# Kernel tuning notes

Measured on AMD Instinct MI355X. Metric: run time of the kernel, lower is better.

The kernel has to match this reference:

```python
import jax, jax.numpy as jnp
import numpy as np

WS = [1024, 2048, 4096, 8192]
RS = [1, 2, 4, 8]
HEAD_IDX = 0
B, N, C, H = 4, 8192, 1024, 128


def setup_inputs() -> dict:
    key = jax.random.key(0)
    kx, kq, kk, kv = jax.random.split(key, 4)
    x = jax.random.normal(kx, (B, N, C), dtype=jnp.float32)
    # small init scale keeps exp(logits) well-conditioned, like trained weights
    Wq = jax.random.normal(kq, (C, H), dtype=jnp.float32) * 0.02
    Wk = jax.random.normal(kk, (C, H), dtype=jnp.float32) * 0.02
    Wv = jax.random.normal(kv, (C, H), dtype=jnp.float32) * 0.02
    return {"x": x, "Wq": Wq, "Wk": Wk, "Wv": Wv}


def _cfg_attention(x, Wq, Wk, Wv, w, r, offset):
    # one (window, dilation) config: strided gather -> causal attn per segment
    b, n, c = x.shape
    h = Wq.shape[1]
    S = n // w
    xs = x.reshape(b, S, w, c)[:, :, offset::r, :]  # [b,S,m,c] dilated sub-seqs
    m = xs.shape[2]
    q = jnp.einsum('bsmc,ch->bsmh', xs, Wq)
    k = jnp.einsum('bsmc,ch->bsmh', xs, Wk)
    v = jnp.einsum('bsmc,ch->bsmh', xs, Wv)
    scores = jnp.einsum('bsqh,bskh->bsqk', q, k) / jnp.sqrt(jnp.float32(h))
    causal = jnp.tril(jnp.ones((m, m), dtype=bool))
    scores = jnp.where(causal, scores, -jnp.inf)
    lse = jax.scipy.special.logsumexp(scores, axis=-1)       # [b,S,m]
    p = jnp.exp(scores - lse[..., None])                     # stable softmax
    o = jnp.einsum('bsqk,bskh->bsqh', p, v)                  # [b,S,m,h]
    denom = jnp.exp(lse)                                     # softmax denominator
    pos = (jnp.arange(S)[:, None] * w + offset
           + jnp.arange(m)[None, :] * r).reshape(-1)         # flat positions [S*m]
    return pos, o.reshape(b, S * m, h), denom.reshape(b, S * m)


def reference(x, Wq, Wk, Wv):
    b, n, _ = x.shape
    h = Wq.shape[1]
    denom_sums = jnp.zeros((b, n), dtype=x.dtype)
    cfgs = []
    for w, r in zip(WS, RS):
        offset = HEAD_IDX % r
        pos, o, denom = _cfg_attention(x, Wq, Wk, Wv, w, r, offset)
        denom_sums = denom_sums.at[:, pos].add(denom)  # cross-config denom sum
        cfgs.append((pos, o, denom))
    out = jnp.zeros((b, n, h), dtype=x.dtype)
    for pos, o, denom in cfgs:
        alpha = denom / denom_sums[:, pos]             # [b, S*m]
        out = out.at[:, pos, :].add(o * alpha[:, :, None])
    return out
```

## Files before the change

kernel.cpp:

```cpp
#include <hip/hip_runtime.h>

typedef __attribute__((ext_vector_type(8))) short s16x8;
typedef __attribute__((ext_vector_type(4))) short s16x4;
typedef __attribute__((ext_vector_type(4))) float f32x4;

#define MFMA16(a,b,c) __builtin_amdgcn_mfma_f32_16x16x32_bf16((a),(b),(c),0,0,0)

#define GLOAD_LDS16(g, l) \
    __builtin_amdgcn_global_load_lds((const __attribute__((address_space(1))) void*)(g), \
                                     (__attribute__((address_space(3))) void*)(l), 16, 0, 0)

__device__ __forceinline__ unsigned short f2bf(float f) {
    unsigned u = __builtin_bit_cast(unsigned, f);
    u = (u + 0x7FFFu + ((u >> 16) & 1u)) >> 16;
    return (unsigned short)u;
}

#define MB ((size_t)1 << 20)
#define WT_OFF   ((size_t)0)
#define QKV_OFF  (1*MB)
#define VT0_OFF  (25*MB)
#define VT1_OFF  (33*MB)
#define VT2_OFF  (37*MB)
#define VT3_OFF  (39*MB)
#define KG1_OFF  (40*MB)
#define KG2_OFF  (44*MB)
#define KG3_OFF  (46*MB)
#define O0_OFF   (47*MB)
#define O1_OFF   (63*MB)
#define O2_OFF   (71*MB)
#define O3_OFF   (75*MB)
#define L0_OFF   (77*MB)
#define L1_OFF   (L0_OFF + (size_t)131072)
#define L2_OFF   (L1_OFF + (size_t)65536)
#define L3_OFF   (L2_OFF + (size_t)32768)

__global__ __launch_bounds__(256) void k_wt(const float* __restrict__ Wq, const float* __restrict__ Wk,
                                            const float* __restrict__ Wv, unsigned short* __restrict__ Wt) {
    int id = blockIdx.x * 256 + threadIdx.x;
    int mat = id >> 17;
    int rem = id & 131071;
    int h = rem >> 10, c = rem & 1023;
    const float* W = (mat == 0) ? Wq : (mat == 1) ? Wk : Wv;
    Wt[id] = f2bf(W[c * 128 + h]);
}

__global__ __launch_bounds__(256, 2) void k_qkv(const float* __restrict__ x,
                                                const unsigned short* __restrict__ Wt,
                                                unsigned short* __restrict__ QKV) {
    union SMem {
        struct { float As[64][64]; unsigned short Bs[384][64]; } s;
        unsigned short Cs[64][392];
    };
    __shared__ SMem sm;
    float* Asf = &sm.s.As[0][0];
    unsigned short* Bsu = &sm.s.Bs[0][0];

    const int mt = blockIdx.x;
    const int tid = threadIdx.x, lane = tid & 63, wv = tid >> 6;
    const int quad = lane >> 4, m16 = lane & 15;
    const int wr = wv >> 1, wc = wv & 1;
    const float* xb = x + (size_t)mt * 64 * 1024;

    f32x4 acc[2][12];
#pragma unroll
    for (int i = 0; i < 2; i++)
#pragma unroll
        for (int j = 0; j < 12; j++) acc[i][j] = (f32x4)0.f;

    for (int kk = 0; kk < 1024; kk += 64) {
#pragma unroll
        for (int t = 0; t < 4; t++) {
            int id = wv * 4 + t;
            int row = id * 4 + (lane >> 4);
            int gl = (lane & 15) ^ (row & 7);
            GLOAD_LDS16(xb + (size_t)row * 1024 + kk + gl * 4, (char*)Asf + id * 1024);
        }
#pragma unroll
        for (int t = 0; t < 12; t++) {
            int id = wv * 12 + t;
            int col = id * 8 + (lane >> 3);
            int gl = (lane & 7) ^ (lane >> 3);
            GLOAD_LDS16(Wt + (size_t)col * 1024 + kk + gl * 8, (char*)Bsu + id * 1024);
        }
        __syncthreads();
#pragma unroll
        for (int c32 = 0; c32 < 2; c32++) {
            s16x8 a[2], b[12];
#pragma unroll
            for (int rt = 0; rt < 2; rt++) {
                int row = wr * 32 + rt * 16 + m16;
                int g0 = c32 * 8 + quad * 2;
                float4 lo = *(const float4*)&Asf[row * 64 + ((g0 ^ (row & 7)) << 2)];
                float4 hi = *(const float4*)&Asf[row * 64 + (((g0 + 1) ^ (row & 7)) << 2)];
                s16x8 av;
                av[0] = (short)f2bf(lo.x); av[1] = (short)f2bf(lo.y);
                av[2] = (short)f2bf(lo.z); av[3] = (short)f2bf(lo.w);
                av[4] = (short)f2bf(hi.x); av[5] = (short)f2bf(hi.y);
                av[6] = (short)f2bf(hi.z); av[7] = (short)f2bf(hi.w);
                a[rt] = av;
            }
#pragma unroll
            for (int ct = 0; ct < 12; ct++) {
                int col = wc * 192 + ct * 16 + m16;
                b[ct] = *(const s16x8*)&Bsu[col * 64 + (((c32 * 4 + quad) ^ (col & 7)) << 3)];
            }
#pragma unroll
            for (int rt = 0; rt < 2; rt++)
#pragma unroll
                for (int ct = 0; ct < 12; ct++) acc[rt][ct] = MFMA16(a[rt], b[ct], acc[rt][ct]);
        }
        __syncthreads();
    }

#pragma unroll
    for (int rt = 0; rt < 2; rt++)
#pragma unroll
        for (int ct = 0; ct < 12; ct++)
#pragma unroll
            for (int rg = 0; rg < 4; rg++)
                sm.Cs[wr * 32 + rt * 16 + quad * 4 + rg][wc * 192 + ct * 16 + m16] = f2bf(acc[rt][ct][rg]);
    __syncthreads();
#pragma unroll
    for (int i = 0; i < 12; i++) {
        int id = tid + 256 * i;
        int row = id / 48, cc = id % 48;
        int col = cc * 8, mat = col >> 7, h = col & 127;
        *(s16x8*)(QKV + (size_t)mat * 4194304 + ((size_t)(mt * 64 + row)) * 128 + h) =
            *(const s16x8*)&sm.Cs[row][col];
    }
}

__device__ __forceinline__ void decode_vt(int bid, int& c, int& b, int& s, int& t8) {
    int base;
    if (bid < 256)      { c = 0; base = 0; }
    else if (bid < 384) { c = 1; base = 256; }
    else if (bid < 448) { c = 2; base = 384; }
    else                { c = 3; base = 448; }
    int rem = bid - base;
    int sh = 6 - c;
    b = rem >> sh;
    int rr = rem & ((1 << sh) - 1);
    s = rr >> 3; t8 = rr & 7;
}

__global__ __launch_bounds__(256) void k_gather(const unsigned short* __restrict__ QKV, char* __restrict__ ws) {
    const unsigned short* K = QKV + (size_t)1 * 4194304;
    const unsigned short* V = QKV + (size_t)2 * 4194304;
    int bid = blockIdx.x, tid = threadIdx.x;
    if (bid < 480) {
        int c, b, s, kb; decode_vt(bid, c, b, s, kb);
        const int S = 8 >> c, r = 1 << c, wseg = 1024 << c;
        const size_t vtoff[4] = {VT0_OFF, VT1_OFF, VT2_OFF, VT3_OFF};
        unsigned short* Vt = (unsigned short*)(ws + vtoff[c]) + ((size_t)(b * S + s)) * 131072;
        int kq8 = tid & 15, hq = tid >> 4;
        int key0 = kb * 128 + kq8 * 8;
        int jt = key0 >> 6, k0 = key0 & 63;
        s16x8 in[8];
#pragma unroll
        for (int i = 0; i < 8; i++) {
            int tok = s * wseg + (key0 + i) * r;
            in[i] = *(const s16x8*)(V + ((size_t)(b * 8192 + tok)) * 128 + hq * 8);
        }
#pragma unroll
        for (int jh = 0; jh < 8; jh++) {
            s16x8 o;
#pragma unroll
            for (int i = 0; i < 8; i++) o[i] = in[i][jh];
            *(s16x8*)(Vt + (size_t)jt * 8192 + (size_t)(hq * 8 + jh) * 64 + k0) = o;
        }
    } else {
        int r2 = bid - 480, c;
        if (r2 < 128)      { c = 1; }
        else if (r2 < 192) { c = 2; r2 -= 128; }
        else               { c = 3; r2 -= 192; }
        const int S = 8 >> c, r = 1 << c, wseg = 1024 << c;
        int b = r2 >> (6 - c);
        int rem = r2 & ((1 << (6 - c)) - 1);
        int s = rem >> 3, kb = rem & 7;
        const size_t kgoff[4] = {0, KG1_OFF, KG2_OFF, KG3_OFF};
        unsigned short* Kg = (unsigned short*)(ws + kgoff[c]) + ((size_t)(b * S + s)) * 131072;
        int row = tid >> 1, hh = (tid & 1) * 64;
        const unsigned short* src = K + ((size_t)(b * 8192 + s * wseg + (kb * 128 + row) * r)) * 128 + hh;
        unsigned short* dst = Kg + ((size_t)(kb * 128 + row)) * 128 + hh;
#pragma unroll
        for (int i = 0; i < 8; i++)
            *(s16x8*)(dst + i * 8) = *(const s16x8*)(src + i * 8);
    }
}

__global__ __launch_bounds__(256, 3) void k_attn(const unsigned short* __restrict__ QKV,
                                                 char* __restrict__ ws) {
    __shared__ s16x8 KsV[1024];
    __shared__ s16x8 VsV[1024];
    __shared__ unsigned short Ps[128][72];

    const int segid = blockIdx.x & 63;
    if (segid >= 60) return;
    const int p = blockIdx.x >> 6;
    int c, b, s;
    if (segid < 32)      { c = 0; b = segid >> 3;        s = segid & 7; }
    else if (segid < 48) { c = 1; b = (segid - 32) >> 2; s = (segid - 32) & 3; }
    else if (segid < 56) { c = 2; b = (segid - 48) >> 1; s = (segid - 48) & 1; }
    else                 { c = 3; b = segid - 56;        s = 0; }
    const int S = 8 >> c, r = 1 << c, wseg = 1024 << c;
    const int segc = b * S + s;
    const int qtL = p, qtH = 15 - p, J = qtH + 1;

    const size_t vtoff[4] = {VT0_OFF, VT1_OFF, VT2_OFF, VT3_OFF};
    const size_t ooff[4]  = {O0_OFF, O1_OFF, O2_OFF, O3_OFF};
    const size_t loff[4]  = {L0_OFF, L1_OFF, L2_OFF, L3_OFF};
    const size_t kgoff[4] = {0, KG1_OFF, KG2_OFF, KG3_OFF};
    const unsigned short* Q  = QKV;
    const unsigned short* Kg = (c == 0)
        ? QKV + (size_t)1 * 4194304 + (size_t)segc * 131072
        : (const unsigned short*)(ws + kgoff[c]) + (size_t)segc * 131072;
    const unsigned short* Vt = (const unsigned short*)(ws + vtoff[c]) + (size_t)segc * 131072;
    float* Ob = (float*)(ws + ooff[c]) + (size_t)segc * 1024 * 128;
    float* Lb = (float*)(ws + loff[c]) + (size_t)segc * 1024;

    const int tid = threadIdx.x, lane = tid & 63, wv = tid >> 6;
    const int quad = lane >> 4, m16 = lane & 15;
    const float SCE = 0.08838834764831845f;

    s16x8 qfL[4], qfH[4];
    {
        int tokL = s * wseg + (qtL * 64 + wv * 16 + m16) * r;
        int tokH = s * wseg + (qtH * 64 + wv * 16 + m16) * r;
        const unsigned short* qpL = Q + ((size_t)(b * 8192 + tokL)) * 128;
        const unsigned short* qpH = Q + ((size_t)(b * 8192 + tokH)) * 128;
#pragma unroll
        for (int c4 = 0; c4 < 4; c4++) {
            qfL[c4] = *(const s16x8*)(qpL + c4 * 32 + quad * 8);
            qfH[c4] = *(const s16x8*)(qpH + c4 * 32 + quad * 8);
        }
    }
    f32x4 oaccL[8], oaccH[8];
#pragma unroll
    for (int i = 0; i < 8; i++) { oaccL[i] = (f32x4)0.f; oaccH[i] = (f32x4)0.f; }
    float lsumL[4] = {}, lsumH[4] = {};

    for (int j = 0; j < J; j++) {
        const unsigned short* Kgt = Kg + (size_t)j * 8192;
        const unsigned short* Vtt = Vt + (size_t)j * 8192;
#pragma unroll
        for (int t = 0; t < 8; t++) {
            int id = wv * 8 + t;
            if (id < 16) {
                int c4 = id >> 2, qd = id & 3;
                GLOAD_LDS16(Kgt + (size_t)lane * 128 + c4 * 32 + qd * 8, &KsV[id * 64]);
            } else {
                int v = id - 16;
                int kc = v >> 3, qd = (v >> 1) & 3, hh = v & 1;
                GLOAD_LDS16(Vtt + (size_t)(hh * 64 + lane) * 64 + kc * 32 + qd * 8,
                            &VsV[(kc * 4 + qd) * 128 + hh * 64]);
            }
        }
        __syncthreads();

        const bool lowA = (j <= qtL);
        const bool dgL = (j == qtL), dgH = (j == qtH);
        const int rbase = wv * 16 + quad * 4;
#pragma unroll
        for (int ct = 0; ct < 4; ct++) {
            f32x4 sL = (f32x4)0.f, sH = (f32x4)0.f;
#pragma unroll
            for (int c4 = 0; c4 < 4; c4++) {
                s16x8 kf = KsV[(c4 * 4 + quad) * 64 + ct * 16 + m16];
                if (lowA) sL = MFMA16(qfL[c4], kf, sL);
                sH = MFMA16(qfH[c4], kf, sH);
            }
            int colL = ct * 16 + m16;
            if (lowA) {
#pragma unroll
                for (int rg = 0; rg < 4; rg++) {
                    float pv = __expf(sL[rg] * SCE);
                    if (dgL && colL > rbase + rg) pv = 0.f;
                    lsumL[rg] += pv;
                    Ps[rbase + rg][colL] = f2bf(pv);
                }
            }
#pragma unroll
            for (int rg = 0; rg < 4; rg++) {
                float pv = __expf(sH[rg] * SCE);
                if (dgH && colL > rbase + rg) pv = 0.f;
                lsumH[rg] += pv;
                Ps[64 + rbase + rg][colL] = f2bf(pv);
            }
        }
#pragma unroll
        for (int kc = 0; kc < 2; kc++) {
            s16x8 aH = *(const s16x8*)&Ps[64 + wv * 16 + m16][kc * 32 + quad * 8];
            s16x8 aL;
            if (lowA) aL = *(const s16x8*)&Ps[wv * 16 + m16][kc * 32 + quad * 8];
#pragma unroll
            for (int nt = 0; nt < 8; nt++) {
                s16x8 bv = VsV[(kc * 4 + quad) * 128 + nt * 16 + m16];
                if (lowA) oaccL[nt] = MFMA16(aL, bv, oaccL[nt]);
                oaccH[nt] = MFMA16(aH, bv, oaccH[nt]);
            }
        }
        __syncthreads();
    }

#pragma unroll
    for (int rg = 0; rg < 4; rg++) {
        float vL = lsumL[rg], vH = lsumH[rg];
        vL += __shfl_xor(vL, 1); vL += __shfl_xor(vL, 2);
        vL += __shfl_xor(vL, 4); vL += __shfl_xor(vL, 8);
        vH += __shfl_xor(vH, 1); vH += __shfl_xor(vH, 2);
        vH += __shfl_xor(vH, 4); vH += __shfl_xor(vH, 8);
        lsumL[rg] = vL; lsumH[rg] = vH;
    }
    float* OcL = Ob + (size_t)(qtL * 64) * 128;
    float* OcH = Ob + (size_t)(qtH * 64) * 128;
#pragma unroll
    for (int nt = 0; nt < 8; nt++)
#pragma unroll
        for (int rg = 0; rg < 4; rg++) {
            int rl = wv * 16 + quad * 4 + rg;
            OcL[(size_t)rl * 128 + nt * 16 + m16] = oaccL[nt][rg];
            OcH[(size_t)rl * 128 + nt * 16 + m16] = oaccH[nt][rg];
        }
    if (m16 == 0) {
#pragma unroll
        for (int rg = 0; rg < 4; rg++) {
            int rl = wv * 16 + quad * 4 + rg;
            Lb[qtL * 64 + rl] = lsumL[rg];
            Lb[qtH * 64 + rl] = lsumH[rg];
        }
    }
}

__global__ __launch_bounds__(256) void k_combine(const char* __restrict__ ws, float* __restrict__ out) {
    int gid = blockIdx.x * 256 + threadIdx.x;
    int rown = gid >> 5;
    int h4 = (gid & 31) * 4;
    int b = rown >> 13, n = rown & 8191;
    const size_t ooff[4] = {O0_OFF, O1_OFF, O2_OFF, O3_OFF};
    const size_t loff[4] = {L0_OFF, L1_OFF, L2_OFF, L3_OFF};
    float denom = 0.f;
    float4 acc = {0.f, 0.f, 0.f, 0.f};
#pragma unroll
    for (int c = 0; c < 4; c++) {
        if ((n & ((1 << c) - 1)) == 0) {
            int s = n >> (10 + c);
            int i = (n & ((1024 << c) - 1)) >> c;
            int rowc = b * (8192 >> c) + (s << 10) + i;
            denom += *((const float*)(ws + loff[c]) + rowc);
            const float4 o = *(const float4*)((const float*)(ws + ooff[c]) + (size_t)rowc * 128 + h4);
            acc.x += o.x; acc.y += o.y; acc.z += o.z; acc.w += o.w;
        }
    }
    float inv = 1.f / denom;
    float4 res = {acc.x * inv, acc.y * inv, acc.z * inv, acc.w * inv};
    *(float4*)(out + (size_t)rown * 128 + h4) = res;
}

extern "C" void kernel_launch(void* const* d_in, const int* in_sizes, int n_in,
                              void* d_out, int out_size, void* d_ws, size_t ws_size,
                              hipStream_t stream) {
    const float* x  = (const float*)d_in[0];
    const float* Wq = (const float*)d_in[1];
    const float* Wk = (const float*)d_in[2];
    const float* Wv = (const float*)d_in[3];
    char* ws = (char*)d_ws;
    unsigned short* Wt  = (unsigned short*)(ws + WT_OFF);
    unsigned short* QKV = (unsigned short*)(ws + QKV_OFF);

    k_wt<<<1536, 256, 0, stream>>>(Wq, Wk, Wv, Wt);
    k_qkv<<<512, 256, 0, stream>>>(x, Wt, QKV);
    k_gather<<<704, 256, 0, stream>>>(QKV, ws);
    k_attn<<<512, 256, 0, stream>>>(QKV, ws);
    k_combine<<<4096, 256, 0, stream>>>(ws, (float*)d_out);
}
```

Before: 297.1 us.

## Drop LDS staging in QKV GEMM and gather strided K directly in attention

The QKV projection stops staging x and the weights through shared memory. Each lane now loads its MFMA fragments straight from global memory, which removes the per-iteration barriers, and occupancy is raised to 3 blocks. Separately, the K-gather copy pass for the dilated configs is removed, and the attention kernel loads strided K rows directly from the QKV buffer into LDS. This saves a kernel phase and workspace traffic, but the GEMM now has no data reuse through LDS and depends on cache hits for the redundant global reads.

New measurement: 450.6 us. +51.7%, slower.

```diff
diff --git a/kernel.cpp b/kernel.cpp
--- a/kernel.cpp
+++ b/kernel.cpp
@@ -23,9 +23,6 @@
 #define VT1_OFF  (33*MB)
 #define VT2_OFF  (37*MB)
 #define VT3_OFF  (39*MB)
-#define KG1_OFF  (40*MB)
-#define KG2_OFF  (44*MB)
-#define KG3_OFF  (46*MB)
 #define O0_OFF   (47*MB)
 #define O1_OFF   (63*MB)
 #define O2_OFF   (71*MB)
@@ -45,17 +42,10 @@
     Wt[id] = f2bf(W[c * 128 + h]);
 }
 
-__global__ __launch_bounds__(256, 2) void k_qkv(const float* __restrict__ x,
+__global__ __launch_bounds__(256, 3) void k_qkv(const float* __restrict__ x,
                                                 const unsigned short* __restrict__ Wt,
                                                 unsigned short* __restrict__ QKV) {
-    union SMem {
-        struct { float As[64][64]; unsigned short Bs[384][64]; } s;
-        unsigned short Cs[64][392];
-    };
-    __shared__ SMem sm;
-    float* Asf = &sm.s.As[0][0];
-    unsigned short* Bsu = &sm.s.Bs[0][0];
-
+    __shared__ unsigned short Cs[64][392];
     const int mt = blockIdx.x;
     const int tid = threadIdx.x, lane = tid & 63, wv = tid >> 6;
     const int quad = lane >> 4, m16 = lane & 15;
@@ -70,29 +60,14 @@
 
     for (int kk = 0; kk < 1024; kk += 64) {
 #pragma unroll
-        for (int t = 0; t < 4; t++) {
-            int id = wv * 4 + t;
-            int row = id * 4 + (lane >> 4);
-            int gl = (lane & 15) ^ (row & 7);
-            GLOAD_LDS16(xb + (size_t)row * 1024 + kk + gl * 4, (char*)Asf + id * 1024);
-        }
-#pragma unroll
-        for (int t = 0; t < 12; t++) {
-            int id = wv * 12 + t;
-            int col = id * 8 + (lane >> 3);
-            int gl = (lane & 7) ^ (lane >> 3);
-            GLOAD_LDS16(Wt + (size_t)col * 1024 + kk + gl * 8, (char*)Bsu + id * 1024);
-        }
-        __syncthreads();
-#pragma unroll
         for (int c32 = 0; c32 < 2; c32++) {
-            s16x8 a[2], b[12];
+            const int k0 = kk + c32 * 32 + quad * 8;
+            s16x8 a[2];
 #pragma unroll
             for (int rt = 0; rt < 2; rt++) {
-                int row = wr * 32 + rt * 16 + m16;
-                int g0 = c32 * 8 + quad * 2;
-                float4 lo = *(const float4*)&Asf[row * 64 + ((g0 ^ (row & 7)) << 2)];
-                float4 hi = *(const float4*)&Asf[row * 64 + (((g0 + 1) ^ (row & 7)) << 2)];
+                const float* ap = xb + (size_t)(wr * 32 + rt * 16 + m16) * 1024 + k0;
+                float4 lo = *(const float4*)ap;
+                float4 hi = *(const float4*)(ap + 4);
                 s16x8 av;
                 av[0] = (short)f2bf(lo.x); av[1] = (short)f2bf(lo.y);
                 av[2] = (short)f2bf(lo.z); av[3] = (short)f2bf(lo.w);
@@ -100,17 +75,15 @@
                 av[6] = (short)f2bf(hi.z); av[7] = (short)f2bf(hi.w);
                 a[rt] = av;
             }
-#pragma unroll
-            for (int ct = 0; ct < 12; ct++) {
-                int col = wc * 192 + ct * 16 + m16;
-                b[ct] = *(const s16x8*)&Bsu[col * 64 + (((c32 * 4 + quad) ^ (col & 7)) << 3)];
-            }
+            s16x8 b[12];
+#pragma unroll
+            for (int ct = 0; ct < 12; ct++)
+                b[ct] = *(const s16x8*)(Wt + (size_t)(wc * 192 + ct * 16 + m16) * 1024 + k0);
 #pragma unroll
             for (int rt = 0; rt < 2; rt++)
 #pragma unroll
                 for (int ct = 0; ct < 12; ct++) acc[rt][ct] = MFMA16(a[rt], b[ct], acc[rt][ct]);
         }
-        __syncthreads();
     }
 
 #pragma unroll
@@ -119,7 +92,7 @@
         for (int ct = 0; ct < 12; ct++)
 #pragma unroll
             for (int rg = 0; rg < 4; rg++)
-                sm.Cs[wr * 32 + rt * 16 + quad * 4 + rg][wc * 192 + ct * 16 + m16] = f2bf(acc[rt][ct][rg]);
+                Cs[wr * 32 + rt * 16 + quad * 4 + rg][wc * 192 + ct * 16 + m16] = f2bf(acc[rt][ct][rg]);
     __syncthreads();
 #pragma unroll
     for (int i = 0; i < 12; i++) {
@@ -127,7 +100,7 @@
         int row = id / 48, cc = id % 48;
         int col = cc * 8, mat = col >> 7, h = col & 127;
         *(s16x8*)(QKV + (size_t)mat * 4194304 + ((size_t)(mt * 64 + row)) * 128 + h) =
-            *(const s16x8*)&sm.Cs[row][col];
+            *(const s16x8*)&Cs[row][col];
     }
 }
 
@@ -145,47 +118,27 @@
 }
 
 __global__ __launch_bounds__(256) void k_gather(const unsigned short* __restrict__ QKV, char* __restrict__ ws) {
-    const unsigned short* K = QKV + (size_t)1 * 4194304;
     const unsigned short* V = QKV + (size_t)2 * 4194304;
     int bid = blockIdx.x, tid = threadIdx.x;
-    if (bid < 480) {
-        int c, b, s, kb; decode_vt(bid, c, b, s, kb);
-        const int S = 8 >> c, r = 1 << c, wseg = 1024 << c;
-        const size_t vtoff[4] = {VT0_OFF, VT1_OFF, VT2_OFF, VT3_OFF};
-        unsigned short* Vt = (unsigned short*)(ws + vtoff[c]) + ((size_t)(b * S + s)) * 131072;
-        int kq8 = tid & 15, hq = tid >> 4;
-        int key0 = kb * 128 + kq8 * 8;
-        int jt = key0 >> 6, k0 = key0 & 63;
-        s16x8 in[8];
-#pragma unroll
-        for (int i = 0; i < 8; i++) {
-            int tok = s * wseg + (key0 + i) * r;
-            in[i] = *(const s16x8*)(V + ((size_t)(b * 8192 + tok)) * 128 + hq * 8);
-        }
-#pragma unroll
-        for (int jh = 0; jh < 8; jh++) {
-            s16x8 o;
-#pragma unroll
-            for (int i = 0; i < 8; i++) o[i] = in[i][jh];
-            *(s16x8*)(Vt + (size_t)jt * 8192 + (size_t)(hq * 8 + jh) * 64 + k0) = o;
-        }
-    } else {
-        int r2 = bid - 480, c;
-        if (r2 < 128)      { c = 1; }
-        else if (r2 < 192) { c = 2; r2 -= 128; }
-        else               { c = 3; r2 -= 192; }
-        const int S = 8 >> c, r = 1 << c, wseg = 1024 << c;
-        int b = r2 >> (6 - c);
-        int rem = r2 & ((1 << (6 - c)) - 1);
-        int s = rem >> 3, kb = rem & 7;
-        const size_t kgoff[4] = {0, KG1_OFF, KG2_OFF, KG3_OFF};
-        unsigned short* Kg = (unsigned short*)(ws + kgoff[c]) + ((size_t)(b * S + s)) * 131072;
-        int row = tid >> 1, hh = (tid & 1) * 64;
-        const unsigned short* src = K + ((size_t)(b * 8192 + s * wseg + (kb * 128 + row) * r)) * 128 + hh;
-        unsigned short* dst = Kg + ((size_t)(kb * 128 + row)) * 128 + hh;
-#pragma unroll
-        for (int i = 0; i < 8; i++)
-            *(s16x8*)(dst + i * 8) = *(const s16x8*)(src + i * 8);
+    int c, b, s, kb; decode_vt(bid, c, b, s, kb);
+    const int S = 8 >> c, r = 1 << c, wseg = 1024 << c;
+    const size_t vtoff[4] = {VT0_OFF, VT1_OFF, VT2_OFF, VT3_OFF};
+    unsigned short* Vt = (unsigned short*)(ws + vtoff[c]) + ((size_t)(b * S + s)) * 131072;
+    int kq8 = tid & 15, hq = tid >> 4;
+    int key0 = kb * 128 + kq8 * 8;
+    int jt = key0 >> 6, k0 = key0 & 63;
+    s16x8 in[8];
+#pragma unroll
+    for (int i = 0; i < 8; i++) {
+        int tok = s * wseg + (key0 + i) * r;
+        in[i] = *(const s16x8*)(V + ((size_t)(b * 8192 + tok)) * 128 + hq * 8);
+    }
+#pragma unroll
+    for (int jh = 0; jh < 8; jh++) {
+        s16x8 o;
+#pragma unroll
+        for (int i = 0; i < 8; i++) o[i] = in[i][jh];
+        *(s16x8*)(Vt + (size_t)jt * 8192 + (size_t)(hq * 8 + jh) * 64 + k0) = o;
     }
 }
 
@@ -210,23 +163,21 @@
     const size_t vtoff[4] = {VT0_OFF, VT1_OFF, VT2_OFF, VT3_OFF};
     const size_t ooff[4]  = {O0_OFF, O1_OFF, O2_OFF, O3_OFF};
     const size_t loff[4]  = {L0_OFF, L1_OFF, L2_OFF, L3_OFF};
-    const size_t kgoff[4] = {0, KG1_OFF, KG2_OFF, KG3_OFF};
     const unsigned short* Q  = QKV;
-    const unsigned short* Kg = (c == 0)
-        ? QKV + (size_t)1 * 4194304 + (size_t)segc * 131072
-        : (const unsigned short*)(ws + kgoff[c]) + (size_t)segc * 131072;
+    const unsigned short* Kb = QKV + (size_t)1 * 4194304 + (size_t)b * 8192 * 128;
     const unsigned short* Vt = (const unsigned short*)(ws + vtoff[c]) + (size_t)segc * 131072;
     float* Ob = (float*)(ws + ooff[c]) + (size_t)segc * 1024 * 128;
     float* Lb = (float*)(ws + loff[c]) + (size_t)segc * 1024;
 
     const int tid = threadIdx.x, lane = tid & 63, wv = tid >> 6;
     const int quad = lane >> 4, m16 = lane & 15;
+    const int sw = s * wseg;
     const float SCE = 0.08838834764831845f;
 
     s16x8 qfL[4], qfH[4];
     {
-        int tokL = s * wseg + (qtL * 64 + wv * 16 + m16) * r;
-        int tokH = s * wseg + (qtH * 64 + wv * 16 + m16) * r;
+        int tokL = sw + (qtL * 64 + wv * 16 + m16) * r;
+        int tokH = sw + (qtH * 64 + wv * 16 + m16) * r;
         const unsigned short* qpL = Q + ((size_t)(b * 8192 + tokL)) * 128;
         const unsigned short* qpH = Q + ((size_t)(b * 8192 + tokH)) * 128;
 #pragma unroll
@@ -241,14 +192,14 @@
     float lsumL[4] = {}, lsumH[4] = {};
 
     for (int j = 0; j < J; j++) {
-        const unsigned short* Kgt = Kg + (size_t)j * 8192;
         const unsigned short* Vtt = Vt + (size_t)j * 8192;
+        const int ktok0 = sw + (j * 64 + lane) * r;
 #pragma unroll
         for (int t = 0; t < 8; t++) {
             int id = wv * 8 + t;
             if (id < 16) {
                 int c4 = id >> 2, qd = id & 3;
-                GLOAD_LDS16(Kgt + (size_t)lane * 128 + c4 * 32 + qd * 8, &KsV[id * 64]);
+                GLOAD_LDS16(Kb + (size_t)ktok0 * 128 + c4 * 32 + qd * 8, &KsV[id * 64]);
             } else {
                 int v = id - 16;
                 int kc = v >> 3, qd = (v >> 1) & 3, hh = v & 1;
@@ -370,7 +321,7 @@
 
     k_wt<<<1536, 256, 0, stream>>>(Wq, Wk, Wv, Wt);
     k_qkv<<<512, 256, 0, stream>>>(x, Wt, QKV);
-    k_gather<<<704, 256, 0, stream>>>(QKV, ws);
+    k_gather<<<480, 256, 0, stream>>>(QKV, ws);
     k_attn<<<512, 256, 0, stream>>>(QKV, ws);
     k_combine<<<4096, 256, 0, stream>>>(ws, (float*)d_out);
 }
```
